# Optimization experiments

Measured on AMD Instinct MI355X. Metric: run time of the kernel, lower is better.

The kernel has to match this reference:

```python
import jax, jax.numpy as jnp
import numpy as np

BS, NQ, D = 4, 12500, 256
HEADS, LEVELS, POINTS = 8, 2, 4
HD = D // HEADS
D_FF = 2048
SHAPES = ((100, 100), (50, 50))   # (H, W) per level; sum(H*W) == NQ
STARTS = (0, 10000)


def layer_norm(x, g, b, eps=1e-5):
    m = x.mean(-1, keepdims=True)
    v = ((x - m) ** 2).mean(-1, keepdims=True)
    return (x - m) * jax.lax.rsqrt(v + eps) * g + b


def bilinear_sample(value_l, loc, H, W):
    # value_l: (bs, heads, H*W, hd); loc: (bs, heads, nq, P, 2) normalized [0,1]
    # matches F.grid_sample(align_corners=False, padding_mode='zeros')
    x = loc[..., 0] * W - 0.5
    y = loc[..., 1] * H - 0.5
    x0 = jnp.floor(x)
    y0 = jnp.floor(y)
    wx1 = x - x0
    wy1 = y - y0
    wx0 = 1.0 - wx1
    wy0 = 1.0 - wy1
    x0i = x0.astype(jnp.int32)
    y0i = y0.astype(jnp.int32)

    def gather(xi, yi):
        valid = (xi >= 0) & (xi < W) & (yi >= 0) & (yi < H)
        idx = jnp.clip(yi, 0, H - 1) * W + jnp.clip(xi, 0, W - 1)  # (bs,heads,nq,P)
        b, h, nq, P = idx.shape
        g = jnp.take_along_axis(value_l, idx.reshape(b, h, nq * P, 1), axis=2)
        g = g.reshape(b, h, nq, P, -1)
        return g * valid[..., None].astype(g.dtype)

    g00 = gather(x0i, y0i)
    g10 = gather(x0i + 1, y0i)
    g01 = gather(x0i, y0i + 1)
    g11 = gather(x0i + 1, y0i + 1)
    return (g00 * (wx0 * wy0)[..., None] + g10 * (wx1 * wy0)[..., None]
            + g01 * (wx0 * wy1)[..., None] + g11 * (wx1 * wy1)[..., None])


def setup_inputs() -> dict:
    key = jax.random.key(0)
    ks = jax.random.split(key, 20)
    s = 0.02
    inp = {
        'query': jax.random.normal(ks[0], (BS, NQ, D), jnp.float32),
        'reference_points': jax.random.uniform(ks[1], (BS, NQ, LEVELS, 2), jnp.float32),
        'w_off': s * jax.random.normal(ks[2], (D, HEADS * LEVELS * POINTS * 2), jnp.float32),
        'b_off': s * jax.random.normal(ks[3], (HEADS * LEVELS * POINTS * 2,), jnp.float32),
        'w_attn': s * jax.random.normal(ks[4], (D, HEADS * LEVELS * POINTS), jnp.float32),
        'b_attn': s * jax.random.normal(ks[5], (HEADS * LEVELS * POINTS,), jnp.float32),
        'w_val': s * jax.random.normal(ks[6], (D, D), jnp.float32),
        'b_val': jnp.zeros((D,), jnp.float32),
        'w_out': s * jax.random.normal(ks[7], (D, D), jnp.float32),
        'b_out': jnp.zeros((D,), jnp.float32),
        'w1': s * jax.random.normal(ks[8], (D, D_FF), jnp.float32),
        'b1': jnp.zeros((D_FF,), jnp.float32),
        'w2': s * jax.random.normal(ks[9], (D_FF, D), jnp.float32),
        'b2': jnp.zeros((D,), jnp.float32),
        'ln0_g': jnp.ones((D,), jnp.float32),
        'ln0_b': jnp.zeros((D,), jnp.float32),
        'ln1_g': jnp.ones((D,), jnp.float32),
        'ln1_b': jnp.zeros((D,), jnp.float32),
    }
    return inp


def reference(query, reference_points, w_off, b_off, w_attn, b_attn, w_val, b_val,
              w_out, b_out, w1, b1, w2, b2, ln0_g, ln0_b, ln1_g, ln1_b):
    bs, nq, _ = query.shape
    # value projection; encoder self-attention: value == query tokens
    value = (query @ w_val + b_val).reshape(bs, nq, HEADS, HD).transpose(0, 2, 1, 3)  # (bs,heads,nv,hd)
    off = (query @ w_off + b_off).reshape(bs, nq, HEADS, LEVELS, POINTS, 2)
    aw = (query @ w_attn + b_attn).reshape(bs, nq, HEADS, LEVELS * POINTS)
    aw = jax.nn.softmax(aw, axis=-1).reshape(bs, nq, HEADS, LEVELS, POINTS)

    out = jnp.zeros((bs, HEADS, nq, HD), query.dtype)
    for l, (H, W) in enumerate(SHAPES):
        normalizer = jnp.array([W, H], query.dtype)
        # (bs,nq,heads,P,2)
        loc = reference_points[:, :, None, l, None, :] + off[:, :, :, l] / normalizer
        loc = loc.transpose(0, 2, 1, 3, 4)  # (bs,heads,nq,P,2)
        v_l = value[:, :, STARTS[l]:STARTS[l] + H * W]  # (bs,heads,H*W,hd)
        sampled = bilinear_sample(v_l, loc, H, W)       # (bs,heads,nq,P,hd)
        w_l = aw[:, :, :, l].transpose(0, 2, 1, 3)      # (bs,heads,nq,P)
        out = out + (sampled * w_l[..., None]).sum(axis=3)

    attn_out = out.transpose(0, 2, 1, 3).reshape(bs, nq, D) @ w_out + b_out
    x = layer_norm(query + attn_out, ln0_g, ln0_b)
    h = jax.nn.relu(x @ w1 + b1)
    x = layer_norm(x + (h @ w2 + b2), ln1_g, ln1_b)
    return x
```

## Files before the change

### kernel.cpp

```cpp
#include <hip/hip_runtime.h>


#define NQv 12500
#define BSv 4
#define Dv  256
#define DFF 2048

typedef __attribute__((ext_vector_type(8))) __bf16 bf16x8;
typedef __attribute__((ext_vector_type(4))) float f32x4;

__device__ __forceinline__ ushort f32_to_bf16(float f) {
  unsigned u = __float_as_uint(f);
  u += 0x7FFFu + ((u >> 16) & 1u);
  return (ushort)(u >> 16);
}
__device__ __forceinline__ float bf16_to_f32(ushort u) {
  return __uint_as_float(((unsigned)u) << 16);
}

__global__ __launch_bounds__(256) void conv_bf16_kernel(
    const float* __restrict__ in, ushort* __restrict__ out, int n4) {
  int i = blockIdx.x * 256 + threadIdx.x;
  if (i >= n4) return;
  float4 v = reinterpret_cast<const float4*>(in)[i];
  uint2 st;
  st.x = (unsigned)f32_to_bf16(v.x) | ((unsigned)f32_to_bf16(v.y) << 16);
  st.y = (unsigned)f32_to_bf16(v.z) | ((unsigned)f32_to_bf16(v.w) << 16);
  reinterpret_cast<uint2*>(out)[i] = st;
}

__global__ __launch_bounds__(256) void ttrans_kernel(
    const float* __restrict__ in, ushort* __restrict__ out, int K, int N) {
  __shared__ ushort tl[64][65];
  const int n0 = blockIdx.x * 64, k0 = blockIdx.y * 64;
  const int t = threadIdx.x;
#pragma unroll
  for (int i = 0; i < 16; ++i) {
    int idx = t + 256 * i;
    int r = idx >> 6, c = idx & 63;
    tl[r][c] = f32_to_bf16(in[(size_t)(k0 + r) * N + n0 + c]);
  }
  __syncthreads();
#pragma unroll
  for (int i = 0; i < 16; ++i) {
    int idx = t + 256 * i;
    int r = idx >> 6, c = idx & 63;
    out[(size_t)(n0 + r) * K + k0 + c] = tl[c][r];
  }
}

__global__ __launch_bounds__(256) void build_wcat_kernel(
    const float* __restrict__ w_val, const float* __restrict__ w_off,
    const float* __restrict__ w_attn, const float* __restrict__ b_val,
    const float* __restrict__ b_off, const float* __restrict__ b_attn,
    ushort* __restrict__ wcat, float* __restrict__ bcat) {
  int i = blockIdx.x * 256 + threadIdx.x;
  if (i < 448 * 256) {
    int n = i >> 8, k = i & 255;
    float v = (n < 256) ? w_val[(size_t)k * 256 + n]
              : (n < 384) ? w_off[(size_t)k * 128 + (n - 256)]
                          : w_attn[(size_t)k * 64 + (n - 384)];
    wcat[i] = f32_to_bf16(v);
  }
  if (i < 512)
    bcat[i] = (i < 256) ? b_val[i] : (i < 384) ? b_off[i - 256]
              : (i < 448) ? b_attn[i - 384] : 0.f;
}

#define TBM 128
#define TBN 128
#define TBK 32

template <int RELU, int NMASK, int SPLIT>
__global__ __launch_bounds__(256) void gemm128_kernel(
    const ushort* __restrict__ A, const ushort* __restrict__ Bt,
    const float* __restrict__ bias, ushort* __restrict__ C,
    ushort* __restrict__ C2,
    int M, int K, int ldc, int Nreal) {
  __shared__ ushort lds[4][TBM * TBK];

  const int t = threadIdx.x;
  const int wid = t >> 6, lane = t & 63;
  const int wr = wid >> 1, wc = wid & 1;
  const int m0 = blockIdx.y * TBM;
  const int n0 = blockIdx.x * TBN;

  int srowA[2], srowB[2], gsl[2];
#pragma unroll
  for (int i = 0; i < 2; i++) {
    int row = i * 64 + (t >> 2);
    int ar = m0 + row;
    srowA[i] = (ar < M) ? ar : (M - 1);
    srowB[i] = n0 + row;
    gsl[i] = ((t & 3) ^ ((row >> 1) & 3)) * 8;
  }

  f32x4 acc[4][4] = {};
  const int nt = K / TBK;
  int cur = 0;

#pragma unroll
  for (int i = 0; i < 2; i++) {
    const int ldsoff = (i * 256 + wid * 64) * 8;
    __builtin_amdgcn_global_load_lds(
        (const __attribute__((address_space(1))) void*)(A + (size_t)srowA[i] * K + gsl[i]),
        (__attribute__((address_space(3))) void*)(lds[0] + ldsoff), 16, 0, 0);
    __builtin_amdgcn_global_load_lds(
        (const __attribute__((address_space(1))) void*)(Bt + (size_t)srowB[i] * K + gsl[i]),
        (__attribute__((address_space(3))) void*)(lds[1] + ldsoff), 16, 0, 0);
  }
  __syncthreads();

  const int rl = lane & 15, kh = lane >> 4;
  for (int tk = 0; tk < nt; ++tk) {
    if (tk + 1 < nt) {
      const int k0 = (tk + 1) * TBK;
      const int nb = (cur ^ 1) * 2;
#pragma unroll
      for (int i = 0; i < 2; i++) {
        const int ldsoff = (i * 256 + wid * 64) * 8;
        __builtin_amdgcn_global_load_lds(
            (const __attribute__((address_space(1))) void*)(A + (size_t)srowA[i] * K + k0 + gsl[i]),
            (__attribute__((address_space(3))) void*)(lds[nb] + ldsoff), 16, 0, 0);
        __builtin_amdgcn_global_load_lds(
            (const __attribute__((address_space(1))) void*)(Bt + (size_t)srowB[i] * K + k0 + gsl[i]),
            (__attribute__((address_space(3))) void*)(lds[nb + 1] + ldsoff), 16, 0, 0);
      }
    }
    {
      const ushort* As = lds[cur * 2];
      const ushort* Bs = lds[cur * 2 + 1];
      bf16x8 afr[4], bfr[4];
#pragma unroll
      for (int ni = 0; ni < 4; ni++) {
        int rowb = wc * 64 + ni * 16 + rl;
        int p = kh ^ ((rowb >> 1) & 3);
        bfr[ni] = *reinterpret_cast<const bf16x8*>(Bs + rowb * 32 + p * 8);
      }
#pragma unroll
      for (int mi = 0; mi < 4; mi++) {
        int rowa = wr * 64 + mi * 16 + rl;
        int p = kh ^ ((rowa >> 1) & 3);
        afr[mi] = *reinterpret_cast<const bf16x8*>(As + rowa * 32 + p * 8);
      }
#pragma unroll
      for (int mi = 0; mi < 4; mi++)
#pragma unroll
        for (int ni = 0; ni < 4; ni++)
          acc[mi][ni] = __builtin_amdgcn_mfma_f32_16x16x32_bf16(afr[mi], bfr[ni], acc[mi][ni], 0, 0, 0);
    }
    __syncthreads();
    cur ^= 1;
  }

  ushort* ldsC = lds[0];
  const int rgrp = lane >> 4, cl = lane & 15;
#pragma unroll
  for (int pass = 0; pass < 2; ++pass) {
    if (wr == pass) {
#pragma unroll
      for (int mi = 0; mi < 4; mi++) {
#pragma unroll
        for (int ni = 0; ni < 4; ni++) {
          int col = wc * 64 + ni * 16 + cl;
          float bv = bias[n0 + col];
#pragma unroll
          for (int r = 0; r < 4; r++) {
            int rloc = mi * 16 + rgrp * 4 + r;
            float v = acc[mi][ni][r] + bv;
            if (RELU) v = fmaxf(v, 0.f);
            ldsC[rloc * 132 + col] = f32_to_bf16(v);
          }
        }
      }
    }
    __syncthreads();
    {
      int rloc = t >> 2;
      int row = m0 + pass * 64 + rloc;
      if (row < M) {
#pragma unroll
        for (int j = 0; j < 4; j++) {
          int col = (t & 3) * 32 + j * 8;
          uint4 v = *reinterpret_cast<const uint4*>(ldsC + rloc * 132 + col);
          if (SPLIT) {
            int gcol = n0 + col;
            if (gcol < 256)
              *reinterpret_cast<uint4*>(C + (size_t)row * 256 + gcol) = v;
            else if (gcol < 448)
              *reinterpret_cast<uint4*>(C2 + (size_t)row * 192 + (gcol - 256)) = v;
          } else if (!NMASK || n0 + col < Nreal) {
            *reinterpret_cast<uint4*>(C + (size_t)row * ldc + n0 + col) = v;
          }
        }
      }
    }
    __syncthreads();
  }
}

__global__ __launch_bounds__(256, 2) void outproj_ln0_kernel(
    const ushort* __restrict__ samp,
    const ushort* __restrict__ wqt,
    const float* __restrict__ bias,
    const float* __restrict__ query,
    const float* __restrict__ g0, const float* __restrict__ be0,
    ushort* __restrict__ xb,
    int M) {
  __shared__ ushort lds_all[32768];
  ushort* As = lds_all;
  ushort* ring0 = lds_all + 16384;

  const int t = threadIdx.x;
  const int wv = t >> 6;
  const int lane = t & 63;
  const int rl = lane & 15, kq = lane >> 4;
  const int cl = lane & 15, g4 = lane >> 4;
  const int m0 = blockIdx.x * 64;

  ushort* ring[2] = {ring0, ring0 + 8192};

  auto issueB = [&](int j, ushort* dst) {
#pragma unroll
    for (int ii = 0; ii < 4; ++ii) {
      int c = t + 256 * ii;
      int s = c >> 8, row = c & 255;
      __builtin_amdgcn_global_load_lds(
          (const __attribute__((address_space(1))) void*)(
              wqt + (size_t)row * 256 + j * 32 + s * 8),
          (__attribute__((address_space(3))) void*)(dst + (size_t)c * 8), 16, 0, 0);
    }
  };

#pragma unroll
  for (int ii = 0; ii < 8; ++ii) {
    int c = t + 256 * ii;
    int s = c >> 6, row = c & 63;
    int ar = m0 + row; ar = (ar < M) ? ar : (M - 1);
    __builtin_amdgcn_global_load_lds(
        (const __attribute__((address_space(1))) void*)(samp + (size_t)ar * 256 + s * 8),
        (__attribute__((address_space(3))) void*)(As + (size_t)c * 8), 16, 0, 0);
  }
  issueB(0, ring[0]);
  __syncthreads();

  f32x4 accF[4][4] = {};
  int cur = 0;

#pragma unroll
  for (int j = 0; j < 8; ++j) {
    if (j + 1 < 8) issueB(j + 1, ring[cur ^ 1]);
    const ushort* Bs = ring[cur];
    bf16x8 afr[4], bfr[4];
#pragma unroll
    for (int mi = 0; mi < 4; mi++)
      afr[mi] = *reinterpret_cast<const bf16x8*>(As + (j * 4 + kq) * 512 + (mi * 16 + rl) * 8);
#pragma unroll
    for (int ni = 0; ni < 4; ni++)
      bfr[ni] = *reinterpret_cast<const bf16x8*>(Bs + kq * 2048 + (wv * 64 + ni * 16 + rl) * 8);
    __builtin_amdgcn_s_setprio(1);
#pragma unroll
    for (int mi = 0; mi < 4; mi++)
#pragma unroll
      for (int ni = 0; ni < 4; ni++)
        accF[mi][ni] = __builtin_amdgcn_mfma_f32_16x16x32_bf16(afr[mi], bfr[ni], accF[mi][ni], 0, 0, 0);
    __builtin_amdgcn_s_setprio(0);
    __syncthreads();
    cur ^= 1;
  }

  float* ptab = (float*)ring0;
  float* mtab = (float*)(ring0 + 2048);

  float bc[4], gc[4], bec[4];
#pragma unroll
  for (int ni = 0; ni < 4; ni++) {
    int col = wv * 64 + ni * 16 + cl;
    bc[ni] = bias[col]; gc[ni] = g0[col]; bec[ni] = be0[col];
  }
#pragma unroll
  for (int mi = 0; mi < 4; mi++) {
#pragma unroll
    for (int ni = 0; ni < 4; ni++) {
      int col = wv * 64 + ni * 16 + cl;
#pragma unroll
      for (int r = 0; r < 4; r++) {
        int row = mi * 16 + g4 * 4 + r;
        int qrow = m0 + row; qrow = (qrow < M) ? qrow : (M - 1);
        accF[mi][ni][r] += bc[ni] + query[(size_t)qrow * 256 + col];
      }
    }
  }
#pragma unroll
  for (int mi = 0; mi < 4; mi++) {
#pragma unroll
    for (int r = 0; r < 4; r++) {
      float s = accF[mi][0][r] + accF[mi][1][r] + accF[mi][2][r] + accF[mi][3][r];
      float sq = accF[mi][0][r] * accF[mi][0][r] + accF[mi][1][r] * accF[mi][1][r] +
                 accF[mi][2][r] * accF[mi][2][r] + accF[mi][3][r] * accF[mi][3][r];
#pragma unroll
      for (int o = 1; o < 16; o <<= 1) {
        s += __shfl_xor(s, o, 64);
        sq += __shfl_xor(sq, o, 64);
      }
      if (cl == 0) {
        int row = mi * 16 + g4 * 4 + r;
        ptab[(row * 4 + wv) * 2 + 0] = s;
        ptab[(row * 4 + wv) * 2 + 1] = sq;
      }
    }
  }
  __syncthreads();
  {
    int row = t >> 2, part = t & 3;
    float s = ptab[(row * 4 + part) * 2 + 0];
    float sq = ptab[(row * 4 + part) * 2 + 1];
    s += __shfl_xor(s, 1, 64);  sq += __shfl_xor(sq, 1, 64);
    s += __shfl_xor(s, 2, 64);  sq += __shfl_xor(sq, 2, 64);
    if (part == 0) {
      float mean = s * (1.f / 256.f);
      float var = sq * (1.f / 256.f) - mean * mean;
      mtab[row * 2 + 0] = mean;
      mtab[row * 2 + 1] = rsqrtf(var + 1e-5f);
    }
  }
  __syncthreads();
#pragma unroll
  for (int mi = 0; mi < 4; mi++) {
#pragma unroll
    for (int r = 0; r < 4; r++) {
      int row = mi * 16 + g4 * 4 + r;
      float2 ms = *reinterpret_cast<const float2*>(mtab + row * 2);
      int grow = m0 + row;
      if (grow < M) {
#pragma unroll
        for (int ni = 0; ni < 4; ni++) {
          int col = wv * 64 + ni * 16 + cl;
          xb[(size_t)grow * 256 + col] =
              f32_to_bf16((accF[mi][ni][r] - ms.x) * ms.y * gc[ni] + bec[ni]);
        }
      }
    }
  }
}

__global__ __launch_bounds__(512, 1) void ffn_ln_fused_kernel(
    const ushort* __restrict__ xb, const ushort* __restrict__ w1t,
    const float* __restrict__ b1, const ushort* __restrict__ w2t,
    const float* __restrict__ b2, const float* __restrict__ g1,
    const float* __restrict__ be1, float* __restrict__ out, int M) {
  __shared__ ushort lds_all[73856];
  ushort* As = lds_all;
  ushort* Hs = lds_all + 32768;
  ushort* stg0 = lds_all + 49280;

  const int t = threadIdx.x;
  const int wv = t >> 6;
  const int wm = wv >> 2;
  const int wn = wv & 3;
  const int lane = t & 63;
  const int rl = lane & 15, kq = lane >> 4;
  const int cl = lane & 15, g4 = lane >> 4;
  const int m0 = blockIdx.x * 128;

  auto stg = [&](int i) { return stg0 + i * 8192; };

  auto issueB1 = [&](int p, int j, ushort* dst) {
#pragma unroll
    for (int ii = 0; ii < 2; ++ii) {
      int c = t + 512 * ii;
      int s = c >> 7, row = c & 127;
      __builtin_amdgcn_global_load_lds(
          (const __attribute__((address_space(1))) void*)(
              w1t + (size_t)(p * 128 + row) * 256 + j * 64 + s * 8),
          (__attribute__((address_space(3))) void*)(dst + (size_t)c * 8), 16, 0, 0);
    }
  };
  auto issueB2 = [&](int p, int tt, ushort* dst) {
#pragma unroll
    for (int ii = 0; ii < 2; ++ii) {
      int c = t + 512 * ii;
      int s = c >> 8, row = c & 255;
      __builtin_amdgcn_global_load_lds(
          (const __attribute__((address_space(1))) void*)(
              w2t + (size_t)row * 2048 + p * 128 + tt * 32 + s * 8),
          (__attribute__((address_space(3))) void*)(dst + (size_t)c * 8), 16, 0, 0);
    }
  };

#pragma unroll
  for (int ii = 0; ii < 8; ++ii) {
    int c = t + 512 * ii;
    int s = c >> 7, row = c & 127;
    int ar = m0 + row; ar = (ar < M) ? ar : (M - 1);
    __builtin_amdgcn_global_load_lds(
        (const __attribute__((address_space(1))) void*)(xb + (size_t)ar * 256 + s * 8),
        (__attribute__((address_space(3))) void*)(As + (size_t)c * 8), 16, 0, 0);
  }
  issueB1(0, 0, stg(0));
  issueB1(0, 1, stg(1));
  asm volatile("s_waitcnt vmcnt(2)" ::: "memory");
  __builtin_amdgcn_s_barrier();

  f32x4 acc1[4][2] = {};
  f32x4 accF[4][4] = {};
  int cur = 0;

  for (int p = 0; p < 16; ++p) {
#pragma unroll
    for (int j = 0; j < 8; ++j) {
      int tgt = cur + 2; if (tgt >= 3) tgt -= 3;
      if (j <= 5) {
        const int j2 = j + 2;
        const int p2 = p + (j2 >> 3);
        if ((j2 & 7) < 4) issueB1(p2, j2 & 3, stg(tgt));
        else issueB2(p2, (j2 & 7) - 4, stg(tgt));
        asm volatile("s_waitcnt vmcnt(4) lgkmcnt(0)" ::: "memory");
      } else if (p < 15) {
        const int j2m = (j + 2) & 7;
        issueB1(p + 1, j2m, stg(tgt));
        asm volatile("s_waitcnt vmcnt(4) lgkmcnt(0)" ::: "memory");
      } else if (j == 6) {
        asm volatile("s_waitcnt vmcnt(2) lgkmcnt(0)" ::: "memory");
      } else {
        asm volatile("s_waitcnt vmcnt(0) lgkmcnt(0)" ::: "memory");
      }
      __builtin_amdgcn_s_barrier();
      __builtin_amdgcn_sched_barrier(0);

      const ushort* Bs = stg(cur);
      if (j < 4) {
        __builtin_amdgcn_s_setprio(1);
#pragma unroll
        for (int kk = 0; kk < 2; ++kk) {
          bf16x8 afr[4], bfr[2];
          const int slotA = j * 8 + kk * 4 + kq;
#pragma unroll
          for (int mi = 0; mi < 4; mi++)
            afr[mi] = *reinterpret_cast<const bf16x8*>(
                As + slotA * 1024 + (wm * 64 + mi * 16 + rl) * 8);
          const int slotB = kk * 4 + kq;
#pragma unroll
          for (int ni = 0; ni < 2; ni++)
            bfr[ni] = *reinterpret_cast<const bf16x8*>(
                Bs + slotB * 1024 + (wn * 32 + ni * 16 + rl) * 8);
#pragma unroll
          for (int mi = 0; mi < 4; mi++)
#pragma unroll
            for (int ni = 0; ni < 2; ni++)
              acc1[mi][ni] = __builtin_amdgcn_mfma_f32_16x16x32_bf16(afr[mi], bfr[ni], acc1[mi][ni], 0, 0, 0);
        }
        __builtin_amdgcn_s_setprio(0);
        if (j == 3) {
#pragma unroll
          for (int ni = 0; ni < 2; ni++) {
            int col = wn * 32 + ni * 16 + cl;
            float b1v = b1[p * 128 + col];
            const int s = col >> 3, w8 = col & 7;
#pragma unroll
            for (int mi = 0; mi < 4; mi++) {
#pragma unroll
              for (int r = 0; r < 4; r++) {
                int row = wm * 64 + mi * 16 + g4 * 4 + r;
                Hs[s * 1032 + row * 8 + w8] = f32_to_bf16(fmaxf(acc1[mi][ni][r] + b1v, 0.f));
              }
            }
          }
#pragma unroll
          for (int mi = 0; mi < 4; mi++)
#pragma unroll
            for (int ni = 0; ni < 2; ni++)
              acc1[mi][ni] = (f32x4){0.f, 0.f, 0.f, 0.f};
        }
      } else {
        const int tt = j - 4;
        bf16x8 a2f[4], b2f[4];
#pragma unroll
        for (int mi = 0; mi < 4; mi++)
          a2f[mi] = *reinterpret_cast<const bf16x8*>(
              Hs + (tt * 4 + kq) * 1032 + (wm * 64 + mi * 16 + rl) * 8);
#pragma unroll
        for (int ni = 0; ni < 4; ni++)
          b2f[ni] = *reinterpret_cast<const bf16x8*>(
              Bs + kq * 2048 + (wn * 64 + ni * 16 + rl) * 8);
        __builtin_amdgcn_s_setprio(1);
#pragma unroll
        for (int mi = 0; mi < 4; mi++)
#pragma unroll
          for (int ni = 0; ni < 4; ni++)
            accF[mi][ni] = __builtin_amdgcn_mfma_f32_16x16x32_bf16(a2f[mi], b2f[ni], accF[mi][ni], 0, 0, 0);
        __builtin_amdgcn_s_setprio(0);
      }
      cur = cur + 1; if (cur >= 3) cur -= 3;
    }
  }

  float* ptab = (float*)stg0;
  float* mtab = (float*)(stg0 + 2048);

  float b2c[4], g1c[4], bec[4];
#pragma unroll
  for (int ni = 0; ni < 4; ni++) {
    int col = wn * 64 + ni * 16 + cl;
    b2c[ni] = b2[col]; g1c[ni] = g1[col]; bec[ni] = be1[col];
  }
#pragma unroll
  for (int mi = 0; mi < 4; mi++) {
#pragma unroll
    for (int ni = 0; ni < 4; ni++) {
      int col = wn * 64 + ni * 16 + cl;
#pragma unroll
      for (int r = 0; r < 4; r++) {
        int row = wm * 64 + mi * 16 + g4 * 4 + r;
        ushort xv = As[(col >> 3) * 1024 + row * 8 + (col & 7)];
        accF[mi][ni][r] += b2c[ni] + bf16_to_f32(xv);
      }
    }
  }
#pragma unroll
  for (int mi = 0; mi < 4; mi++) {
#pragma unroll
    for (int r = 0; r < 4; r++) {
      float s = accF[mi][0][r] + accF[mi][1][r] + accF[mi][2][r] + accF[mi][3][r];
      float sq = accF[mi][0][r] * accF[mi][0][r] + accF[mi][1][r] * accF[mi][1][r] +
                 accF[mi][2][r] * accF[mi][2][r] + accF[mi][3][r] * accF[mi][3][r];
#pragma unroll
      for (int o = 1; o < 16; o <<= 1) {
        s += __shfl_xor(s, o, 64);
        sq += __shfl_xor(sq, o, 64);
      }
      if (cl == 0) {
        int row = wm * 64 + mi * 16 + g4 * 4 + r;
        ptab[(row * 4 + wn) * 2 + 0] = s;
        ptab[(row * 4 + wn) * 2 + 1] = sq;
      }
    }
  }
  __syncthreads();
  {
    int row = t >> 2, part = t & 3;
    float s = ptab[(row * 4 + part) * 2 + 0];
    float sq = ptab[(row * 4 + part) * 2 + 1];
    s += __shfl_xor(s, 1, 64);  sq += __shfl_xor(sq, 1, 64);
    s += __shfl_xor(s, 2, 64);  sq += __shfl_xor(sq, 2, 64);
    if (part == 0) {
      float mean = s * (1.f / 256.f);
      float var = sq * (1.f / 256.f) - mean * mean;
      mtab[row * 2 + 0] = mean;
      mtab[row * 2 + 1] = rsqrtf(var + 1e-5f);
    }
  }
  __syncthreads();
#pragma unroll
  for (int mi = 0; mi < 4; mi++) {
#pragma unroll
    for (int r = 0; r < 4; r++) {
      int row = wm * 64 + mi * 16 + g4 * 4 + r;
      float2 ms = *reinterpret_cast<const float2*>(mtab + row * 2);
      int grow = m0 + row;
      if (grow < M) {
#pragma unroll
        for (int ni = 0; ni < 4; ni++) {
          int col = wn * 64 + ni * 16 + cl;
          out[(size_t)grow * 256 + col] = (accF[mi][ni][r] - ms.x) * ms.y * g1c[ni] + bec[ni];
        }
      }
    }
  }
}

__global__ __launch_bounds__(256) void deform_attn_kernel(
    const ushort* __restrict__ val,
    const ushort* __restrict__ oa,
    const float* __restrict__ refp,
    ushort* __restrict__ out,
    int total)
{
  int tid = blockIdx.x * 256 + threadIdx.x;
  if (tid >= total) return;
  int c = tid & 3;
  int idx = tid >> 2;
  int h = idx & 7;
  int row = idx >> 3;
  int bl = row / NQv;

  const ushort* orow = oa + (size_t)row * 192;

  uint lraw = *reinterpret_cast<const uint*>(orow + 128 + h * 8 + c * 2);
  float l0 = bf16_to_f32((ushort)(lraw & 0xffffu));
  float l1 = bf16_to_f32((ushort)(lraw >> 16));
  float mx = fmaxf(l0, l1);
  mx = fmaxf(mx, __shfl_xor(mx, 1, 64));
  mx = fmaxf(mx, __shfl_xor(mx, 2, 64));
  float e0 = __expf(l0 - mx), e1 = __expf(l1 - mx);
  float sm = e0 + e1;
  sm += __shfl_xor(sm, 1, 64);
  sm += __shfl_xor(sm, 2, 64);
  float inv = 1.f / sm;

  ushort o4[4];
  *reinterpret_cast<uint2*>(o4) = *reinterpret_cast<const uint2*>(orow + h * 16 + c * 4);
  float4 rp = *reinterpret_cast<const float4*>(refp + (size_t)row * 4);
  float Wl = (c & 2) ? 50.f : 100.f;
  float fx = ((c & 2) ? rp.z : rp.x) * Wl - 0.5f;
  float fy = ((c & 2) ? rp.w : rp.y) * Wl - 0.5f;
  float myx0 = fx + bf16_to_f32(o4[0]);
  float myy0 = fy + bf16_to_f32(o4[1]);
  float myx1 = fx + bf16_to_f32(o4[2]);
  float myy1 = fy + bf16_to_f32(o4[3]);
  float myw0 = e0 * inv, myw1 = e1 * inv;

  const int lanebase = (threadIdx.x & 63) & ~3;
  float acc8[8] = {};
#pragma unroll
  for (int p = 0; p < 8; ++p) {
    const int src = lanebase | (p >> 1);
    float x = __shfl((p & 1) ? myx1 : myx0, src, 64);
    float y = __shfl((p & 1) ? myy1 : myy0, src, 64);
    float w = __shfl((p & 1) ? myw1 : myw0, src, 64);
    const int W = (p < 4) ? 100 : 50, H = W;
    const ushort* vbase = val + ((size_t)bl * NQv + ((p < 4) ? 0 : 10000)) * 256 + h * 32 + c * 8;
    float x0f = floorf(x), y0f = floorf(y);
    float wx1 = x - x0f, wy1 = y - y0f;
    float wx0 = 1.f - wx1, wy0 = 1.f - wy1;
    int x0 = (int)x0f, y0 = (int)y0f;
    float cw[4] = {w * wx0 * wy0, w * wx1 * wy0, w * wx0 * wy1, w * wx1 * wy1};
    int cx[4] = {x0, x0 + 1, x0, x0 + 1};
    int cy[4] = {y0, y0, y0 + 1, y0 + 1};
#pragma unroll
    for (int cc = 0; cc < 4; cc++) {
      int xi = cx[cc], yi = cy[cc];
      if (xi >= 0 && xi < W && yi >= 0 && yi < H) {
        ushort vr[8];
        *reinterpret_cast<uint4*>(vr) =
            *reinterpret_cast<const uint4*>(vbase + (size_t)(yi * W + xi) * 256);
        float ww = cw[cc];
#pragma unroll
        for (int j = 0; j < 8; j++) acc8[j] += ww * bf16_to_f32(vr[j]);
      }
    }
  }

  ushort st[8];
#pragma unroll
  for (int j = 0; j < 8; j++) st[j] = f32_to_bf16(acc8[j]);
  *reinterpret_cast<uint4*>(out + (size_t)row * 256 + h * 32 + c * 8) =
      *reinterpret_cast<uint4*>(st);
}

extern "C" void kernel_launch(void* const* d_in, const int* in_sizes, int n_in,
                              void* d_out, int out_size, void* d_ws, size_t ws_size,
                              hipStream_t stream) {
  const float* query  = (const float*)d_in[0];
  const float* refp   = (const float*)d_in[1];
  const float* w_off  = (const float*)d_in[2];
  const float* b_off  = (const float*)d_in[3];
  const float* w_attn = (const float*)d_in[4];
  const float* b_attn = (const float*)d_in[5];
  const float* w_val  = (const float*)d_in[6];
  const float* b_val  = (const float*)d_in[7];
  const float* w_out  = (const float*)d_in[8];
  const float* b_out  = (const float*)d_in[9];
  const float* w1     = (const float*)d_in[10];
  const float* b1     = (const float*)d_in[11];
  const float* w2     = (const float*)d_in[12];
  const float* b2     = (const float*)d_in[13];
  const float* ln0g   = (const float*)d_in[14];
  const float* ln0b   = (const float*)d_in[15];
  const float* ln1g   = (const float*)d_in[16];
  const float* ln1b   = (const float*)d_in[17];
  float* outp = (float*)d_out;

  char* ws = (char*)d_ws;
  size_t woff = 0;
  auto walloc = [&](size_t bytes) { size_t r = woff; woff += (bytes + 255) & ~(size_t)255; return r; };
  ushort* wcat = (ushort*)(ws + walloc((size_t)512 * 256 * 2));
  float*  bcat = (float*)(ws + walloc(512 * 4));
  ushort* wqt  = (ushort*)(ws + walloc((size_t)256 * 256 * 2));
  ushort* w1t  = (ushort*)(ws + walloc((size_t)DFF * 256 * 2));
  ushort* w2t  = (ushort*)(ws + walloc((size_t)256 * DFF * 2));
  char* arena = ws + woff;
  size_t arena_sz = (ws_size > woff) ? (ws_size - woff) : 0;

  int nb = ((size_t)BSv * NQv * 1920 + (1u << 20) <= arena_sz) ? BSv : 1;
  const int R = nb * NQv;
  ushort* qb   = (ushort*)arena;
  ushort* valb = (ushort*)(arena + (size_t)R * 512);
  ushort* oab  = (ushort*)(arena + (size_t)R * 1024);
  ushort* samp = (ushort*)(arena + (size_t)R * 1408);
  ushort* xb   = qb;

  build_wcat_kernel<<<dim3(448), dim3(256), 0, stream>>>(
      w_val, w_off, w_attn, b_val, b_off, b_attn, wcat, bcat);
  ttrans_kernel<<<dim3(4, 4), dim3(256), 0, stream>>>(w_out, wqt, Dv, Dv);
  ttrans_kernel<<<dim3(DFF / 64, 4), dim3(256), 0, stream>>>(w1, w1t, Dv, DFF);
  ttrans_kernel<<<dim3(4, DFF / 64), dim3(256), 0, stream>>>(w2, w2t, DFF, Dv);

  const int MT = (R + TBM - 1) / TBM;

  for (int c = 0; c < BSv / nb; c++) {
    const int row0 = c * R;
    const float* qrow = query + (size_t)row0 * Dv;

    conv_bf16_kernel<<<dim3((R * 64 + 255) / 256), dim3(256), 0, stream>>>(qrow, qb, R * 64);

    gemm128_kernel<0, 1, 1><<<dim3(4, MT), dim3(256), 0, stream>>>(
        qb, wcat, bcat, valb, oab, R, Dv, 448, 448);

    deform_attn_kernel<<<dim3((R * 32 + 255) / 256), dim3(256), 0, stream>>>(
        valb, oab, refp + (size_t)row0 * 4, samp, R * 32);

    outproj_ln0_kernel<<<dim3((R + 63) / 64), dim3(256), 0, stream>>>(
        samp, wqt, b_out, qrow, ln0g, ln0b, xb, R);

    ffn_ln_fused_kernel<<<dim3((R + 127) / 128), dim3(512), 0, stream>>>(
        xb, w1t, b1, w2t, b2, ln1g, ln1b, outp + (size_t)row0 * 256, R);
  }
}
```

Measured before the change: 363.1 us.

## Store weights and intermediates in LDS-tile-native blocked layouts for contiguous staging loads

Adds a staging-format kernel that rearranges the transposed weights (w_out, w1, w2) into per-tile contiguous blocks matching the LDS layout. The deform-attn output and the outproj/LN0 output are also written in blocked tile order, so the next kernel can copy each tile with fully contiguous global_load_lds addresses. This is meant to cut scattered, strided global loads when filling LDS. In exchange the scattered writes move to the producer kernels: xb is now written as 2-byte elements with a 1024-element stride, which may coalesce poorly. The workspace also needs padded buffers.

Result: faster. 332.0 us (-8.6%).

```diff
diff --git a/kernel.cpp b/kernel.cpp
--- a/kernel.cpp
+++ b/kernel.cpp
@@ -65,6 +65,20 @@
   if (i < 512)
     bcat[i] = (i < 256) ? b_val[i] : (i < 384) ? b_off[i - 256]
               : (i < 448) ? b_attn[i - 384] : 0.f;
+}
+
+template <int MODE>
+__global__ __launch_bounds__(256) void stagefmt_kernel(
+    const ushort* __restrict__ src, ushort* __restrict__ dst) {
+  int i = blockIdx.x * 256 + threadIdx.x;
+  int g = i >> 10, c = i & 1023;
+  int srcrow, srck;
+  if (MODE == 0) { srcrow = (g >> 2) * 128 + (c & 127); srck = (g & 3) * 64 + ((c >> 7) & 7) * 8; }
+  if (MODE == 1) { srcrow = c & 255; srck = (g >> 2) * 128 + (g & 3) * 32 + ((c >> 8) & 3) * 8; }
+  if (MODE == 2) { srcrow = c & 255; srck = g * 32 + ((c >> 8) & 3) * 8; }
+  const int LD = (MODE == 1) ? 2048 : 256;
+  *reinterpret_cast<uint4*>(dst + (size_t)i * 8) =
+      *reinterpret_cast<const uint4*>(src + (size_t)srcrow * LD + srck);
 }
 
 #define TBM 128
@@ -201,7 +215,7 @@
 
 __global__ __launch_bounds__(256, 2) void outproj_ln0_kernel(
     const ushort* __restrict__ samp,
-    const ushort* __restrict__ wqt,
+    const ushort* __restrict__ wqf,
     const float* __restrict__ bias,
     const float* __restrict__ query,
     const float* __restrict__ g0, const float* __restrict__ be0,
@@ -224,10 +238,8 @@
 #pragma unroll
     for (int ii = 0; ii < 4; ++ii) {
       int c = t + 256 * ii;
-      int s = c >> 8, row = c & 255;
       __builtin_amdgcn_global_load_lds(
-          (const __attribute__((address_space(1))) void*)(
-              wqt + (size_t)row * 256 + j * 32 + s * 8),
+          (const __attribute__((address_space(1))) void*)(wqf + (size_t)j * 8192 + (size_t)c * 8),
           (__attribute__((address_space(3))) void*)(dst + (size_t)c * 8), 16, 0, 0);
     }
   };
@@ -235,10 +247,9 @@
 #pragma unroll
   for (int ii = 0; ii < 8; ++ii) {
     int c = t + 256 * ii;
-    int s = c >> 6, row = c & 63;
-    int ar = m0 + row; ar = (ar < M) ? ar : (M - 1);
     __builtin_amdgcn_global_load_lds(
-        (const __attribute__((address_space(1))) void*)(samp + (size_t)ar * 256 + s * 8),
+        (const __attribute__((address_space(1))) void*)(
+            samp + (size_t)blockIdx.x * 16384 + (size_t)c * 8),
         (__attribute__((address_space(3))) void*)(As + (size_t)c * 8), 16, 0, 0);
   }
   issueB(0, ring[0]);
@@ -333,10 +344,11 @@
       float2 ms = *reinterpret_cast<const float2*>(mtab + row * 2);
       int grow = m0 + row;
       if (grow < M) {
+        size_t base = (size_t)(grow >> 7) * 32768 + (size_t)(grow & 127) * 8;
 #pragma unroll
         for (int ni = 0; ni < 4; ni++) {
           int col = wv * 64 + ni * 16 + cl;
-          xb[(size_t)grow * 256 + col] =
+          xb[base + (size_t)(col >> 3) * 1024 + (col & 7)] =
               f32_to_bf16((accF[mi][ni][r] - ms.x) * ms.y * gc[ni] + bec[ni]);
         }
       }
@@ -345,10 +357,13 @@
 }
 
 __global__ __launch_bounds__(512, 1) void ffn_ln_fused_kernel(
-    const ushort* __restrict__ xb, const ushort* __restrict__ w1t,
-    const float* __restrict__ b1, const ushort* __restrict__ w2t,
-    const float* __restrict__ b2, const float* __restrict__ g1,
-    const float* __restrict__ be1, float* __restrict__ out, int M) {
+    const ushort* __restrict__ xb,
+    const ushort* __restrict__ w1f,
+    const float* __restrict__ b1,
+    const ushort* __restrict__ w2f,
+    const float* __restrict__ b2,
+    const float* __restrict__ g1, const float* __restrict__ be1,
+    float* __restrict__ out, int M) {
   __shared__ ushort lds_all[73856];
   ushort* As = lds_all;
   ushort* Hs = lds_all + 32768;
@@ -366,24 +381,22 @@
   auto stg = [&](int i) { return stg0 + i * 8192; };
 
   auto issueB1 = [&](int p, int j, ushort* dst) {
+    const ushort* src = w1f + (size_t)(p * 4 + j) * 8192;
 #pragma unroll
     for (int ii = 0; ii < 2; ++ii) {
       int c = t + 512 * ii;
-      int s = c >> 7, row = c & 127;
       __builtin_amdgcn_global_load_lds(
-          (const __attribute__((address_space(1))) void*)(
-              w1t + (size_t)(p * 128 + row) * 256 + j * 64 + s * 8),
+          (const __attribute__((address_space(1))) void*)(src + (size_t)c * 8),
           (__attribute__((address_space(3))) void*)(dst + (size_t)c * 8), 16, 0, 0);
     }
   };
   auto issueB2 = [&](int p, int tt, ushort* dst) {
+    const ushort* src = w2f + (size_t)(p * 4 + tt) * 8192;
 #pragma unroll
     for (int ii = 0; ii < 2; ++ii) {
       int c = t + 512 * ii;
-      int s = c >> 8, row = c & 255;
       __builtin_amdgcn_global_load_lds(
-          (const __attribute__((address_space(1))) void*)(
-              w2t + (size_t)row * 2048 + p * 128 + tt * 32 + s * 8),
+          (const __attribute__((address_space(1))) void*)(src + (size_t)c * 8),
           (__attribute__((address_space(3))) void*)(dst + (size_t)c * 8), 16, 0, 0);
     }
   };
@@ -391,10 +404,9 @@
 #pragma unroll
   for (int ii = 0; ii < 8; ++ii) {
     int c = t + 512 * ii;
-    int s = c >> 7, row = c & 127;
-    int ar = m0 + row; ar = (ar < M) ? ar : (M - 1);
     __builtin_amdgcn_global_load_lds(
-        (const __attribute__((address_space(1))) void*)(xb + (size_t)ar * 256 + s * 8),
+        (const __attribute__((address_space(1))) void*)(
+            xb + (size_t)blockIdx.x * 32768 + (size_t)c * 8),
         (__attribute__((address_space(3))) void*)(As + (size_t)c * 8), 16, 0, 0);
   }
   issueB1(0, 0, stg(0));
@@ -644,7 +656,8 @@
   ushort st[8];
 #pragma unroll
   for (int j = 0; j < 8; j++) st[j] = f32_to_bf16(acc8[j]);
-  *reinterpret_cast<uint4*>(out + (size_t)row * 256 + h * 32 + c * 8) =
+  *reinterpret_cast<uint4*>(out + (size_t)(row >> 6) * 16384 +
+                            (size_t)(h * 4 + c) * 512 + (size_t)(row & 63) * 8) =
       *reinterpret_cast<uint4*>(st);
 }
 
@@ -679,15 +692,20 @@
   ushort* wqt  = (ushort*)(ws + walloc((size_t)256 * 256 * 2));
   ushort* w1t  = (ushort*)(ws + walloc((size_t)DFF * 256 * 2));
   ushort* w2t  = (ushort*)(ws + walloc((size_t)256 * DFF * 2));
+  ushort* wqf  = (ushort*)(ws + walloc((size_t)8 * 8192 * 2));
+  ushort* w1f  = (ushort*)(ws + walloc((size_t)64 * 8192 * 2));
+  ushort* w2f  = (ushort*)(ws + walloc((size_t)64 * 8192 * 2));
   char* arena = ws + woff;
   size_t arena_sz = (ws_size > woff) ? (ws_size - woff) : 0;
 
-  int nb = ((size_t)BSv * NQv * 1920 + (1u << 20) <= arena_sz) ? BSv : 1;
+  int nb = ((size_t)BSv * NQv * 1920 + (4u << 20) <= arena_sz) ? BSv : 1;
   const int R = nb * NQv;
+  const size_t xbsz = (size_t)((R + 127) / 128) * 65536;
+  const size_t smsz = (size_t)((R + 63) / 64) * 32768;
   ushort* qb   = (ushort*)arena;
-  ushort* valb = (ushort*)(arena + (size_t)R * 512);
-  ushort* oab  = (ushort*)(arena + (size_t)R * 1024);
-  ushort* samp = (ushort*)(arena + (size_t)R * 1408);
+  ushort* valb = (ushort*)(arena + xbsz);
+  ushort* oab  = (ushort*)(arena + xbsz + (size_t)R * 512);
+  ushort* samp = (ushort*)(arena + xbsz + (size_t)R * 512 + (size_t)R * 384);
   ushort* xb   = qb;
 
   build_wcat_kernel<<<dim3(448), dim3(256), 0, stream>>>(
@@ -695,6 +713,9 @@
   ttrans_kernel<<<dim3(4, 4), dim3(256), 0, stream>>>(w_out, wqt, Dv, Dv);
   ttrans_kernel<<<dim3(DFF / 64, 4), dim3(256), 0, stream>>>(w1, w1t, Dv, DFF);
   ttrans_kernel<<<dim3(4, DFF / 64), dim3(256), 0, stream>>>(w2, w2t, DFF, Dv);
+  stagefmt_kernel<2><<<dim3(32), dim3(256), 0, stream>>>(wqt, wqf);
+  stagefmt_kernel<0><<<dim3(256), dim3(256), 0, stream>>>(w1t, w1f);
+  stagefmt_kernel<1><<<dim3(256), dim3(256), 0, stream>>>(w2t, w2f);
 
   const int MT = (R + TBM - 1) / TBM;
 
@@ -711,9 +732,9 @@
         valb, oab, refp + (size_t)row0 * 4, samp, R * 32);
 
     outproj_ln0_kernel<<<dim3((R + 63) / 64), dim3(256), 0, stream>>>(
-        samp, wqt, b_out, qrow, ln0g, ln0b, xb, R);
+        samp, wqf, b_out, qrow, ln0g, ln0b, xb, R);
 
     ffn_ln_fused_kernel<<<dim3((R + 127) / 128), dim3(512), 0, stream>>>(
-        xb, w1t, b1, w2t, b2, ln1g, ln1b, outp + (size_t)row0 * 256, R);
-  }
-}
+        xb, w1f, b1, w2f, b2, ln1g, ln1b, outp + (size_t)row0 * 256, R);
+  }
+}
```
